# Performance work log

Measured on AMD Instinct MI355X. Metric: run time of the kernel, lower is better.

The kernel has to match this reference:

```python
import jax, jax.numpy as jnp
import numpy as np

B, S, H = 1, 1024, 2880
NQ, NKV, D = 64, 8, 64          # query heads, kv heads, head_dim
G = NQ // NKV                    # GQA group size
W = 128                          # sliding window
SCALE = D ** -0.5
NEG = -1e30


def rotate_half(x):
    x1, x2 = jnp.split(x, 2, axis=-1)
    return jnp.concatenate((-x2, x1), axis=-1)


def setup_inputs() -> dict:
    key = jax.random.key(0)
    ks = jax.random.split(key, 8)
    hidden_states = jax.random.normal(ks[0], (B, S, H), jnp.float32)
    # rotary tables, half head_dim (module concats (cos,cos) to full dim)
    pos = jnp.arange(S, dtype=jnp.float32)[:, None]
    inv = 1.0 / (10000.0 ** (jnp.arange(0, D, 2, dtype=jnp.float32) / D))
    ang = pos * inv[None, :]                      # (S, D/2)
    cos = jnp.cos(ang)[None].astype(jnp.float32)  # (1, S, D/2)
    sin = jnp.sin(ang)[None].astype(jnp.float32)
    w_qkv = jax.random.normal(ks[1], (H, (NQ + 2 * NKV) * D), jnp.float32) * 0.02
    b_qkv = jax.random.normal(ks[2], ((NQ + 2 * NKV) * D,), jnp.float32) * 0.02
    w_o = jax.random.normal(ks[3], (NQ * D, H), jnp.float32) * 0.02
    b_o = jax.random.normal(ks[4], (H,), jnp.float32) * 0.02
    sinks = jax.random.normal(ks[5], (NQ,), jnp.float32)
    k_cache = jnp.zeros((B, S, NKV, D), jnp.float32)
    v_cache = jnp.zeros((B, S, NKV, D), jnp.float32)
    return {"hidden_states": hidden_states, "cos": cos, "sin": sin,
            "w_qkv": w_qkv, "b_qkv": b_qkv, "w_o": w_o, "b_o": b_o,
            "sinks": sinks, "k_cache": k_cache, "v_cache": v_cache, "kv_len": 0}


def reference(hidden_states, cos, sin, w_qkv, b_qkv, w_o, b_o, sinks,
              k_cache, v_cache, kv_len):
    # fused QKV projection + split
    qkv = hidden_states @ w_qkv + b_qkv                      # (B, S, (NQ+2*NKV)*D)
    q, k, v = jnp.split(qkv, [NQ * D, NQ * D + NKV * D], axis=-1)
    q = q.reshape(B, S, NQ, D)
    k = k.reshape(B, S, NKV, D)
    v = v.reshape(B, S, NKV, D)
    # RoPE (BSND layout, half-dim tables duplicated to full dim)
    cosf = jnp.concatenate((cos, cos), axis=-1)[:, :, None, :]
    sinf = jnp.concatenate((sin, sin), axis=-1)[:, :, None, :]
    q = q * cosf + rotate_half(q) * sinf
    k = k * cosf + rotate_half(k) * sinf
    # KV-cache scatter update at position kv_len along seq dim
    k_cache = jax.lax.dynamic_update_slice(k_cache, k, (0, kv_len, 0, 0))
    v_cache = jax.lax.dynamic_update_slice(v_cache, v, (0, kv_len, 0, 0))
    T = kv_len + S
    keys = k_cache[:, :T]                                    # (B, T, NKV, D)
    vals = v_cache[:, :T]
    # GQA: group query heads by kv head
    qg = q.reshape(B, S, NKV, G, D)
    scores = jnp.einsum('bqhgd,bkhd->bhgqk', qg, keys) * SCALE  # (B,NKV,G,S,T)
    # causal + sliding-window mask
    i = jnp.arange(S)[:, None] + kv_len
    j = jnp.arange(T)[None, :]
    allowed = (j <= i) & (i - j < W)
    scores = jnp.where(allowed, scores, NEG)
    # softmax with per-head learnable sink logit (sink gets no value)
    sk = sinks.reshape(NKV, G)[None, :, :, None]             # (1,NKV,G,1)
    m = jnp.maximum(jnp.max(scores, axis=-1), sk)            # (B,NKV,G,S)
    p = jnp.exp(scores - m[..., None])
    denom = jnp.sum(p, axis=-1) + jnp.exp(sk - m)
    attn = jnp.einsum('bhgqk,bkhd->bqhgd', p / denom[..., None], vals)
    out = attn.reshape(B, S, NQ * D) @ w_o + b_o             # (B, S, H)
    return out
```

## Files before the change

### kernel.cpp

```cpp
#include <hip/hip_runtime.h>
#include <hip/hip_bf16.h>

#define NQH 64
#define NKVH 8
#define DH 64
#define SEQ 1024
#define HID 2880
#define QKV_N 5120
#define ATTN_N 4096
#define WIN 128
#define WO_NPAD 2944
#define SCALE_F 0.125f

typedef __attribute__((ext_vector_type(8))) __bf16 bf16x8;
typedef __attribute__((ext_vector_type(4))) float f32x4;

#define GLOAD_LDS16(g, l) \
    __builtin_amdgcn_global_load_lds((const __attribute__((address_space(1))) void*)(g), \
                                     (__attribute__((address_space(3))) void*)(l), 16, 0, 0)

__device__ __forceinline__ ushort f2bf(float x) {
    union { float f; unsigned int u; } c; c.f = x;
    unsigned int u = c.u;
    unsigned int r = (u + 0x7FFFu + ((u >> 16) & 1u)) >> 16;
    return (ushort)r;
}

__global__ __launch_bounds__(256) void convert_f32_bf16(
    const float* __restrict__ in, ushort* __restrict__ out, int n4)
{
    int idx = blockIdx.x * blockDim.x + threadIdx.x;
    int stride = gridDim.x * blockDim.x;
    for (int i = idx; i < n4; i += stride) {
        float4 v = reinterpret_cast<const float4*>(in)[i];
        ushort4 o;
        o.x = f2bf(v.x); o.y = f2bf(v.y); o.z = f2bf(v.z); o.w = f2bf(v.w);
        reinterpret_cast<ushort4*>(out)[i] = o;
    }
}

__global__ __launch_bounds__(256) void transpose_convert(
    const float* __restrict__ in, ushort* __restrict__ out, int K, int N)
{
    __shared__ ushort tile[64][80];
    const int bk = blockIdx.x * 64;
    const int bn = blockIdx.y * 64;
    const int tid = threadIdx.x;
    const bool inb = bn < N;

#pragma unroll
    for (int it = 0; it < 4; ++it) {
        int r = it * 16 + (tid >> 4);
        int c4 = (tid & 15) * 4;
        float4 v = make_float4(0.f, 0.f, 0.f, 0.f);
        if (inb) v = *(const float4*)&in[(size_t)(bk + r) * N + bn + c4];
        tile[c4 + 0][r] = f2bf(v.x);
        tile[c4 + 1][r] = f2bf(v.y);
        tile[c4 + 2][r] = f2bf(v.z);
        tile[c4 + 3][r] = f2bf(v.w);
    }
    __syncthreads();
#pragma unroll
    for (int it = 0; it < 2; ++it) {
        int nr = it * 32 + (tid >> 3);
        int c8 = (tid & 7) * 8;
        uint4 v = *(const uint4*)&tile[nr][c8];
        *(uint4*)&out[(size_t)(bn + nr) * K + bk + c8] = v;
    }
}

template<bool ROPE>
__global__ __launch_bounds__(256) void gemm64x128(
    const ushort* __restrict__ A, const ushort* __restrict__ BT,
    const float* __restrict__ bias, float* __restrict__ C,
    int K, int ldC, int Nreal,
    const float* __restrict__ cosp, const float* __restrict__ sinp)
{
    __shared__ ushort Al[2 * 64 * 64];
    __shared__ ushort Bl[2 * 128 * 64];
    const int t = threadIdx.x;
    const int lane = t & 63;
    const int w = t >> 6;
    const int wr = w >> 1, wc = w & 1;
    const int g4 = lane >> 4;
    const int r15 = lane & 15;

    const int flat = blockIdx.x + gridDim.x * blockIdx.y;
    const int per = (gridDim.x * gridDim.y) >> 3;
    const int virt = (flat & 7) * per + (flat >> 3);
    const int m0 = (virt & 15) * 64;
    const int n0 = (virt >> 4) * 128;

    const ushort* aSrc0; const ushort* aSrc1;
    ushort* aDst0; ushort* aDst1;
    {
        int lin0 = t, lin1 = 256 + t;
        int row0 = lin0 >> 3, row1 = lin1 >> 3;
        int ch0 = (lin0 & 7) ^ (row0 & 7);
        int ch1 = (lin1 & 7) ^ (row1 & 7);
        aSrc0 = A + (size_t)(m0 + row0) * K + ch0 * 8;
        aSrc1 = A + (size_t)(m0 + row1) * K + ch1 * 8;
        aDst0 = &Al[lin0 * 8];
        aDst1 = &Al[lin1 * 8];
    }
    const ushort* bSrc0; const ushort* bSrc1; const ushort* bSrc2; const ushort* bSrc3;
    ushort* bDst0; ushort* bDst1; ushort* bDst2; ushort* bDst3;
    {
        int lin;
        lin = t;       bSrc0 = BT + (size_t)(n0 + (lin >> 3)) * K + (((lin & 7) ^ ((lin >> 3) & 7)) * 8); bDst0 = &Bl[lin * 8];
        lin = 256 + t; bSrc1 = BT + (size_t)(n0 + (lin >> 3)) * K + (((lin & 7) ^ ((lin >> 3) & 7)) * 8); bDst1 = &Bl[lin * 8];
        lin = 512 + t; bSrc2 = BT + (size_t)(n0 + (lin >> 3)) * K + (((lin & 7) ^ ((lin >> 3) & 7)) * 8); bDst2 = &Bl[lin * 8];
        lin = 768 + t; bSrc3 = BT + (size_t)(n0 + (lin >> 3)) * K + (((lin & 7) ^ ((lin >> 3) & 7)) * 8); bDst3 = &Bl[lin * 8];
    }

#define STAGE_TILE(bufsel) do { \
        GLOAD_LDS16(aSrc0, aDst0 + (bufsel) * 4096); \
        GLOAD_LDS16(aSrc1, aDst1 + (bufsel) * 4096); \
        GLOAD_LDS16(bSrc0, bDst0 + (bufsel) * 8192); \
        GLOAD_LDS16(bSrc1, bDst1 + (bufsel) * 8192); \
        GLOAD_LDS16(bSrc2, bDst2 + (bufsel) * 8192); \
        GLOAD_LDS16(bSrc3, bDst3 + (bufsel) * 8192); \
        aSrc0 += 64; aSrc1 += 64; \
        bSrc0 += 64; bSrc1 += 64; bSrc2 += 64; bSrc3 += 64; \
    } while (0)

    int aoff[2][2], boff[4][2];
#pragma unroll
    for (int mi = 0; mi < 2; ++mi)
#pragma unroll
        for (int ks = 0; ks < 2; ++ks) {
            int row = wr * 32 + mi * 16 + r15;
            int slot = (ks * 4 + g4) ^ (row & 7);
            aoff[mi][ks] = row * 64 + slot * 8;
        }
#pragma unroll
    for (int ni = 0; ni < 4; ++ni)
#pragma unroll
        for (int ks = 0; ks < 2; ++ks) {
            int col = wc * 64 + ni * 16 + r15;
            int slot = (ks * 4 + g4) ^ (col & 7);
            boff[ni][ks] = col * 64 + slot * 8;
        }

    f32x4 acc[2][4];
#pragma unroll
    for (int mi = 0; mi < 2; ++mi)
#pragma unroll
        for (int ni = 0; ni < 4; ++ni) acc[mi][ni] = (f32x4){0.f, 0.f, 0.f, 0.f};

#define COMPUTE_TILE(bufsel) do { \
        const ushort* Ab = &Al[(bufsel) * 4096]; \
        const ushort* Bb = &Bl[(bufsel) * 8192]; \
        _Pragma("unroll") \
        for (int ks = 0; ks < 2; ++ks) { \
            bf16x8 a0 = *(const bf16x8*)&Ab[aoff[0][ks]]; \
            bf16x8 a1 = *(const bf16x8*)&Ab[aoff[1][ks]]; \
            bf16x8 b0 = *(const bf16x8*)&Bb[boff[0][ks]]; \
            bf16x8 b1 = *(const bf16x8*)&Bb[boff[1][ks]]; \
            bf16x8 b2 = *(const bf16x8*)&Bb[boff[2][ks]]; \
            bf16x8 b3 = *(const bf16x8*)&Bb[boff[3][ks]]; \
            __builtin_amdgcn_s_setprio(1); \
            acc[0][0] = __builtin_amdgcn_mfma_f32_16x16x32_bf16(a0, b0, acc[0][0], 0, 0, 0); \
            acc[0][1] = __builtin_amdgcn_mfma_f32_16x16x32_bf16(a0, b1, acc[0][1], 0, 0, 0); \
            acc[0][2] = __builtin_amdgcn_mfma_f32_16x16x32_bf16(a0, b2, acc[0][2], 0, 0, 0); \
            acc[0][3] = __builtin_amdgcn_mfma_f32_16x16x32_bf16(a0, b3, acc[0][3], 0, 0, 0); \
            acc[1][0] = __builtin_amdgcn_mfma_f32_16x16x32_bf16(a1, b0, acc[1][0], 0, 0, 0); \
            acc[1][1] = __builtin_amdgcn_mfma_f32_16x16x32_bf16(a1, b1, acc[1][1], 0, 0, 0); \
            acc[1][2] = __builtin_amdgcn_mfma_f32_16x16x32_bf16(a1, b2, acc[1][2], 0, 0, 0); \
            acc[1][3] = __builtin_amdgcn_mfma_f32_16x16x32_bf16(a1, b3, acc[1][3], 0, 0, 0); \
            __builtin_amdgcn_s_setprio(0); \
        } \
    } while (0)

    const int NT = K >> 6;
    STAGE_TILE(0);
    for (int kt = 0; kt < NT; kt += 2) {
        if (kt + 1 < NT) {
            STAGE_TILE(1);
            asm volatile("s_waitcnt vmcnt(6)" ::: "memory");
        } else {
            asm volatile("s_waitcnt vmcnt(0)" ::: "memory");
        }
        __builtin_amdgcn_s_barrier();
        COMPUTE_TILE(0);
        asm volatile("s_waitcnt lgkmcnt(0)" ::: "memory");
        __builtin_amdgcn_s_barrier();
        if (kt + 1 < NT) {
            if (kt + 2 < NT) {
                STAGE_TILE(0);
                asm volatile("s_waitcnt vmcnt(6)" ::: "memory");
            } else {
                asm volatile("s_waitcnt vmcnt(0)" ::: "memory");
            }
            __builtin_amdgcn_s_barrier();
            COMPUTE_TILE(1);
            asm volatile("s_waitcnt lgkmcnt(0)" ::: "memory");
            __builtin_amdgcn_s_barrier();
        }
    }
#undef STAGE_TILE
#undef COMPUTE_TILE

    float vals[2][4][4];
#pragma unroll
    for (int ni = 0; ni < 4; ++ni) {
        int col = n0 + wc * 64 + ni * 16 + r15;
        float bv = (col < Nreal) ? bias[col] : 0.f;
#pragma unroll
        for (int mi = 0; mi < 2; ++mi)
#pragma unroll
            for (int r = 0; r < 4; ++r) vals[mi][ni][r] = acc[mi][ni][r] + bv;
    }
    if (ROPE) {
        const int head = (n0 + wc * 64) >> 6;
        if (head < 72) {
#pragma unroll
            for (int mi = 0; mi < 2; ++mi)
#pragma unroll
                for (int r = 0; r < 4; ++r) {
                    int q = m0 + wr * 32 + mi * 16 + g4 * 4 + r;
#pragma unroll
                    for (int dp = 0; dp < 2; ++dp) {
                        int d = dp * 16 + r15;
                        float c = cosp[q * 32 + d];
                        float s = sinp[q * 32 + d];
                        float x1 = vals[mi][dp][r];
                        float x2 = vals[mi][dp + 2][r];
                        vals[mi][dp][r]     = x1 * c - x2 * s;
                        vals[mi][dp + 2][r] = x2 * c + x1 * s;
                    }
                }
        }
    }
#pragma unroll
    for (int ni = 0; ni < 4; ++ni) {
        int col = n0 + wc * 64 + ni * 16 + r15;
        if (col < Nreal) {
#pragma unroll
            for (int mi = 0; mi < 2; ++mi) {
                int row = m0 + wr * 32 + mi * 16 + g4 * 4;
#pragma unroll
                for (int r = 0; r < 4; ++r)
                    C[(size_t)(row + r) * ldC + col] = vals[mi][ni][r];
            }
        }
    }
}

__global__ __launch_bounds__(512) void attn_mfma_kernel(
    const float* __restrict__ qkv, const float* __restrict__ sinks,
    ushort* __restrict__ attn_out)
{
    __shared__ __align__(16) ushort Kl[160][72];
    __shared__ __align__(16) ushort Vt[64][168];
    __shared__ __align__(16) ushort Pl[8][32][40];
    const int t = threadIdx.x;
    const int w = t >> 6;
    const int l = t & 63;
    const int g4 = l >> 4;
    const int r15 = l & 15;
    const int q0 = blockIdx.x * 32;
    const int hk = blockIdx.y;
    const int kbase = q0 - 128;

#pragma unroll
    for (int i = 0; i < 5; ++i) {
        int idx = i * 512 + t;
        int row = idx >> 4;
        int c4 = (idx & 15) * 4;
        int j = kbase + row;
        float4 kv = make_float4(0.f, 0.f, 0.f, 0.f);
        float4 vv = make_float4(0.f, 0.f, 0.f, 0.f);
        if (j >= 0) {
            kv = *(const float4*)&qkv[(size_t)j * QKV_N + 4096 + hk * 64 + c4];
            vv = *(const float4*)&qkv[(size_t)j * QKV_N + 4608 + hk * 64 + c4];
        }
        ushort4 kp;
        kp.x = f2bf(kv.x); kp.y = f2bf(kv.y); kp.z = f2bf(kv.z); kp.w = f2bf(kv.w);
        *(ushort4*)&Kl[row][c4] = kp;
        Vt[c4 + 0][row] = f2bf(vv.x);
        Vt[c4 + 1][row] = f2bf(vv.y);
        Vt[c4 + 2][row] = f2bf(vv.z);
        Vt[c4 + 3][row] = f2bf(vv.w);
    }

    bf16x8 qf[2][2];
#pragma unroll
    for (int ct = 0; ct < 2; ++ct) {
        int R = w * 32 + ct * 16 + r15;
        int q = q0 + (R & 31);
        int hq = hk * 8 + (R >> 5);
        const float* qb = &qkv[(size_t)q * QKV_N + hq * 64];
#pragma unroll
        for (int s = 0; s < 2; ++s) {
            float4 a = *(const float4*)&qb[s * 32 + g4 * 8];
            float4 b = *(const float4*)&qb[s * 32 + g4 * 8 + 4];
            union { ushort u[8]; bf16x8 v; } pk;
            pk.u[0] = f2bf(a.x * SCALE_F); pk.u[1] = f2bf(a.y * SCALE_F);
            pk.u[2] = f2bf(a.z * SCALE_F); pk.u[3] = f2bf(a.w * SCALE_F);
            pk.u[4] = f2bf(b.x * SCALE_F); pk.u[5] = f2bf(b.y * SCALE_F);
            pk.u[6] = f2bf(b.z * SCALE_F); pk.u[7] = f2bf(b.w * SCALE_F);
            qf[ct][s] = pk.v;
        }
    }
    __syncthreads();

    f32x4 sc[10][2];
#pragma unroll
    for (int kt = 0; kt < 10; ++kt) {
        sc[kt][0] = (f32x4){0.f, 0.f, 0.f, 0.f};
        sc[kt][1] = (f32x4){0.f, 0.f, 0.f, 0.f};
    }
#pragma unroll
    for (int kt = 0; kt < 10; ++kt) {
#pragma unroll
        for (int s = 0; s < 2; ++s) {
            bf16x8 kf = *(const bf16x8*)&Kl[kt * 16 + r15][s * 32 + g4 * 8];
            sc[kt][0] = __builtin_amdgcn_mfma_f32_16x16x32_bf16(kf, qf[0][s], sc[kt][0], 0, 0, 0);
            sc[kt][1] = __builtin_amdgcn_mfma_f32_16x16x32_bf16(kf, qf[1][s], sc[kt][1], 0, 0, 0);
        }
    }

    const int minkey = 128 - q0;
#pragma unroll
    for (int ct = 0; ct < 2; ++ct) {
        int R = w * 32 + ct * 16 + r15;
        int ql = R & 31;
        float snk = sinks[hk * 8 + (R >> 5)];
#pragma unroll
        for (int kt = 0; kt < 10; ++kt)
#pragma unroll
            for (int r = 0; r < 4; ++r) {
                int key = kt * 16 + g4 * 4 + r;
                bool ok = (key > ql) && (key <= ql + 128) && (key >= minkey);
                if (!ok) sc[kt][ct][r] = -1e30f;
            }
        float m = snk;
#pragma unroll
        for (int kt = 0; kt < 10; ++kt)
#pragma unroll
            for (int r = 0; r < 4; ++r) m = fmaxf(m, sc[kt][ct][r]);
        m = fmaxf(m, __shfl_xor(m, 16));
        m = fmaxf(m, __shfl_xor(m, 32));
        float sum = 0.f;
#pragma unroll
        for (int kt = 0; kt < 10; ++kt)
#pragma unroll
            for (int r = 0; r < 4; ++r) {
                float p = __expf(sc[kt][ct][r] - m);
                sc[kt][ct][r] = p;
                sum += p;
            }
        sum += __shfl_xor(sum, 16);
        sum += __shfl_xor(sum, 32);
        sum += __expf(snk - m);
        float iv = 1.0f / sum;
#pragma unroll
        for (int kt = 0; kt < 10; ++kt)
#pragma unroll
            for (int r = 0; r < 4; ++r) sc[kt][ct][r] *= iv;
    }

    f32x4 pv[2][4];
#pragma unroll
    for (int mi = 0; mi < 2; ++mi)
#pragma unroll
        for (int ni = 0; ni < 4; ++ni) pv[mi][ni] = (f32x4){0.f, 0.f, 0.f, 0.f};

#pragma unroll
    for (int s = 0; s < 5; ++s) {
#pragma unroll
        for (int ct = 0; ct < 2; ++ct)
#pragma unroll
            for (int kh = 0; kh < 2; ++kh) {
                int kt = 2 * s + kh;
                ushort4 p4;
                p4.x = f2bf(sc[kt][ct][0]);
                p4.y = f2bf(sc[kt][ct][1]);
                p4.z = f2bf(sc[kt][ct][2]);
                p4.w = f2bf(sc[kt][ct][3]);
                *(ushort4*)&Pl[w][ct * 16 + r15][kh * 16 + g4 * 4] = p4;
            }
#pragma unroll
        for (int mi = 0; mi < 2; ++mi) {
            bf16x8 pf = *(const bf16x8*)&Pl[w][mi * 16 + r15][g4 * 8];
#pragma unroll
            for (int ni = 0; ni < 4; ++ni) {
                bf16x8 vf = *(const bf16x8*)&Vt[ni * 16 + r15][s * 32 + g4 * 8];
                pv[mi][ni] = __builtin_amdgcn_mfma_f32_16x16x32_bf16(pf, vf, pv[mi][ni], 0, 0, 0);
            }
        }
    }

#pragma unroll
    for (int mi = 0; mi < 2; ++mi)
#pragma unroll
        for (int r = 0; r < 4; ++r) {
            int R = w * 32 + mi * 16 + g4 * 4 + r;
            int q = q0 + (R & 31);
            int hq = hk * 8 + (R >> 5);
            ushort* ob = &attn_out[(size_t)q * ATTN_N + hq * 64 + r15];
#pragma unroll
            for (int ni = 0; ni < 4; ++ni)
                ob[ni * 16] = f2bf(pv[mi][ni][r]);
        }
}

extern "C" void kernel_launch(void* const* d_in, const int* in_sizes, int n_in,
                              void* d_out, int out_size, void* d_ws, size_t ws_size,
                              hipStream_t stream)
{
    const float* hidden = (const float*)d_in[0];
    const float* cosp   = (const float*)d_in[1];
    const float* sinp   = (const float*)d_in[2];
    const float* w_qkv  = (const float*)d_in[3];
    const float* b_qkv  = (const float*)d_in[4];
    const float* w_o    = (const float*)d_in[5];
    const float* b_o    = (const float*)d_in[6];
    const float* sinks  = (const float*)d_in[7];

    char* ws = (char*)d_ws;
    size_t off = 0;
    ushort* wqkvT = (ushort*)(ws + off); off += (size_t)QKV_N * HID * 2;
    ushort* woT   = (ushort*)(ws + off); off += (size_t)WO_NPAD * ATTN_N * 2;
    float*  qkv   = (float*)(ws + off);  off += (size_t)SEQ * QKV_N * 4;
    ushort* hidden_b = (ushort*)(ws + off);
    ushort* attn_b   = (ushort*)(ws + off); off += (size_t)SEQ * ATTN_N * 2;
    if (off > ws_size) return;

    transpose_convert<<<dim3(HID / 64, QKV_N / 64), 256, 0, stream>>>(w_qkv, wqkvT, HID, QKV_N);
    transpose_convert<<<dim3(ATTN_N / 64, WO_NPAD / 64), 256, 0, stream>>>(w_o, woT, ATTN_N, HID);
    convert_f32_bf16<<<2048, 256, 0, stream>>>(hidden, hidden_b, SEQ * HID / 4);

    gemm64x128<true><<<dim3(QKV_N / 128, SEQ / 64), 256, 0, stream>>>(
        hidden_b, wqkvT, b_qkv, qkv, HID, QKV_N, QKV_N, cosp, sinp);

    attn_mfma_kernel<<<dim3(SEQ / 32, NKVH), 512, 0, stream>>>(qkv, sinks, attn_b);

    gemm64x128<false><<<dim3(WO_NPAD / 128, SEQ / 64), 256, 0, stream>>>(
        attn_b, woT, b_o, (float*)d_out, ATTN_N, HID, HID, nullptr, nullptr);
}
```

Baseline: 151.9 us.

## Enlarge GEMM block tile to 128x128 with eight waves per block

Both GEMMs now use 128x128 output tiles computed by 512-thread blocks (8 waves, each still 32x64), replacing the 64x128 tile with 4 waves. Each block loads A and B tiles with two LDS-direct loads per operand per thread, which raises reuse of the B tile across more rows. The change also removes s_setprio around the MFMA bursts and inserts sched_barriers around the compute sections. The grid halves in block count, which risks lower occupancy or poorer load balance across CUs, especially for the output projection with 23 column tiles.

```diff
diff --git a/kernel.cpp b/kernel.cpp
--- a/kernel.cpp
+++ b/kernel.cpp
@@ -70,58 +70,48 @@
 }
 
 template<bool ROPE>
-__global__ __launch_bounds__(256) void gemm64x128(
+__global__ __launch_bounds__(512) void gemm128w8(
     const ushort* __restrict__ A, const ushort* __restrict__ BT,
     const float* __restrict__ bias, float* __restrict__ C,
     int K, int ldC, int Nreal,
     const float* __restrict__ cosp, const float* __restrict__ sinp)
 {
-    __shared__ ushort Al[2 * 64 * 64];
-    __shared__ ushort Bl[2 * 128 * 64];
+    __shared__ ushort Al[2 * 8192];
+    __shared__ ushort Bl[2 * 8192];
     const int t = threadIdx.x;
     const int lane = t & 63;
     const int w = t >> 6;
-    const int wr = w >> 1, wc = w & 1;
+    const int wr = w >> 1;
+    const int wc = w & 1;
     const int g4 = lane >> 4;
     const int r15 = lane & 15;
 
     const int flat = blockIdx.x + gridDim.x * blockIdx.y;
     const int per = (gridDim.x * gridDim.y) >> 3;
     const int virt = (flat & 7) * per + (flat >> 3);
-    const int m0 = (virt & 15) * 64;
-    const int n0 = (virt >> 4) * 128;
-
-    const ushort* aSrc0; const ushort* aSrc1;
-    ushort* aDst0; ushort* aDst1;
+    const int m0 = (virt & 7) * 128;
+    const int n0 = (virt >> 3) * 128;
+
+    const ushort *aS0, *aS1, *bS0, *bS1;
+    int dO0, dO1;
     {
-        int lin0 = t, lin1 = 256 + t;
+        int lin0 = t, lin1 = 512 + t;
         int row0 = lin0 >> 3, row1 = lin1 >> 3;
         int ch0 = (lin0 & 7) ^ (row0 & 7);
         int ch1 = (lin1 & 7) ^ (row1 & 7);
-        aSrc0 = A + (size_t)(m0 + row0) * K + ch0 * 8;
-        aSrc1 = A + (size_t)(m0 + row1) * K + ch1 * 8;
-        aDst0 = &Al[lin0 * 8];
-        aDst1 = &Al[lin1 * 8];
-    }
-    const ushort* bSrc0; const ushort* bSrc1; const ushort* bSrc2; const ushort* bSrc3;
-    ushort* bDst0; ushort* bDst1; ushort* bDst2; ushort* bDst3;
-    {
-        int lin;
-        lin = t;       bSrc0 = BT + (size_t)(n0 + (lin >> 3)) * K + (((lin & 7) ^ ((lin >> 3) & 7)) * 8); bDst0 = &Bl[lin * 8];
-        lin = 256 + t; bSrc1 = BT + (size_t)(n0 + (lin >> 3)) * K + (((lin & 7) ^ ((lin >> 3) & 7)) * 8); bDst1 = &Bl[lin * 8];
-        lin = 512 + t; bSrc2 = BT + (size_t)(n0 + (lin >> 3)) * K + (((lin & 7) ^ ((lin >> 3) & 7)) * 8); bDst2 = &Bl[lin * 8];
-        lin = 768 + t; bSrc3 = BT + (size_t)(n0 + (lin >> 3)) * K + (((lin & 7) ^ ((lin >> 3) & 7)) * 8); bDst3 = &Bl[lin * 8];
-    }
-
-#define STAGE_TILE(bufsel) do { \
-        GLOAD_LDS16(aSrc0, aDst0 + (bufsel) * 4096); \
-        GLOAD_LDS16(aSrc1, aDst1 + (bufsel) * 4096); \
-        GLOAD_LDS16(bSrc0, bDst0 + (bufsel) * 8192); \
-        GLOAD_LDS16(bSrc1, bDst1 + (bufsel) * 8192); \
-        GLOAD_LDS16(bSrc2, bDst2 + (bufsel) * 8192); \
-        GLOAD_LDS16(bSrc3, bDst3 + (bufsel) * 8192); \
-        aSrc0 += 64; aSrc1 += 64; \
-        bSrc0 += 64; bSrc1 += 64; bSrc2 += 64; bSrc3 += 64; \
+        aS0 = A  + (size_t)(m0 + row0) * K + ch0 * 8;
+        aS1 = A  + (size_t)(m0 + row1) * K + ch1 * 8;
+        bS0 = BT + (size_t)(n0 + row0) * K + ch0 * 8;
+        bS1 = BT + (size_t)(n0 + row1) * K + ch1 * 8;
+        dO0 = lin0 * 8; dO1 = lin1 * 8;
+    }
+
+#define STAGE_TILE(buf) do { \
+        GLOAD_LDS16(aS0, &Al[(buf) * 8192 + dO0]); \
+        GLOAD_LDS16(aS1, &Al[(buf) * 8192 + dO1]); \
+        GLOAD_LDS16(bS0, &Bl[(buf) * 8192 + dO0]); \
+        GLOAD_LDS16(bS1, &Bl[(buf) * 8192 + dO1]); \
+        aS0 += 64; aS1 += 64; bS0 += 64; bS1 += 64; \
     } while (0)
 
     int aoff[2][2], boff[4][2];
@@ -148,9 +138,9 @@
 #pragma unroll
         for (int ni = 0; ni < 4; ++ni) acc[mi][ni] = (f32x4){0.f, 0.f, 0.f, 0.f};
 
-#define COMPUTE_TILE(bufsel) do { \
-        const ushort* Ab = &Al[(bufsel) * 4096]; \
-        const ushort* Bb = &Bl[(bufsel) * 8192]; \
+#define COMPUTE_TILE(buf) do { \
+        const ushort* Ab = &Al[(buf) * 8192]; \
+        const ushort* Bb = &Bl[(buf) * 8192]; \
         _Pragma("unroll") \
         for (int ks = 0; ks < 2; ++ks) { \
             bf16x8 a0 = *(const bf16x8*)&Ab[aoff[0][ks]]; \
@@ -159,7 +149,6 @@
             bf16x8 b1 = *(const bf16x8*)&Bb[boff[1][ks]]; \
             bf16x8 b2 = *(const bf16x8*)&Bb[boff[2][ks]]; \
             bf16x8 b3 = *(const bf16x8*)&Bb[boff[3][ks]]; \
-            __builtin_amdgcn_s_setprio(1); \
             acc[0][0] = __builtin_amdgcn_mfma_f32_16x16x32_bf16(a0, b0, acc[0][0], 0, 0, 0); \
             acc[0][1] = __builtin_amdgcn_mfma_f32_16x16x32_bf16(a0, b1, acc[0][1], 0, 0, 0); \
             acc[0][2] = __builtin_amdgcn_mfma_f32_16x16x32_bf16(a0, b2, acc[0][2], 0, 0, 0); \
@@ -168,7 +157,6 @@
             acc[1][1] = __builtin_amdgcn_mfma_f32_16x16x32_bf16(a1, b1, acc[1][1], 0, 0, 0); \
             acc[1][2] = __builtin_amdgcn_mfma_f32_16x16x32_bf16(a1, b2, acc[1][2], 0, 0, 0); \
             acc[1][3] = __builtin_amdgcn_mfma_f32_16x16x32_bf16(a1, b3, acc[1][3], 0, 0, 0); \
-            __builtin_amdgcn_s_setprio(0); \
         } \
     } while (0)
 
@@ -177,31 +165,34 @@
     for (int kt = 0; kt < NT; kt += 2) {
         if (kt + 1 < NT) {
             STAGE_TILE(1);
-            asm volatile("s_waitcnt vmcnt(6)" ::: "memory");
+            asm volatile("s_waitcnt vmcnt(4)" ::: "memory");
         } else {
             asm volatile("s_waitcnt vmcnt(0)" ::: "memory");
         }
         __builtin_amdgcn_s_barrier();
+        __builtin_amdgcn_sched_barrier(0);
         COMPUTE_TILE(0);
         asm volatile("s_waitcnt lgkmcnt(0)" ::: "memory");
+        __builtin_amdgcn_sched_barrier(0);
         __builtin_amdgcn_s_barrier();
         if (kt + 1 < NT) {
             if (kt + 2 < NT) {
                 STAGE_TILE(0);
-                asm volatile("s_waitcnt vmcnt(6)" ::: "memory");
+                asm volatile("s_waitcnt vmcnt(4)" ::: "memory");
             } else {
                 asm volatile("s_waitcnt vmcnt(0)" ::: "memory");
             }
             __builtin_amdgcn_s_barrier();
+            __builtin_amdgcn_sched_barrier(0);
             COMPUTE_TILE(1);
             asm volatile("s_waitcnt lgkmcnt(0)" ::: "memory");
+            __builtin_amdgcn_sched_barrier(0);
             __builtin_amdgcn_s_barrier();
         }
     }
 #undef STAGE_TILE
 #undef COMPUTE_TILE
 
-    float vals[2][4][4];
 #pragma unroll
     for (int ni = 0; ni < 4; ++ni) {
         int col = n0 + wc * 64 + ni * 16 + r15;
@@ -209,7 +200,7 @@
 #pragma unroll
         for (int mi = 0; mi < 2; ++mi)
 #pragma unroll
-            for (int r = 0; r < 4; ++r) vals[mi][ni][r] = acc[mi][ni][r] + bv;
+            for (int r = 0; r < 4; ++r) acc[mi][ni][r] += bv;
     }
     if (ROPE) {
         const int head = (n0 + wc * 64) >> 6;
@@ -224,10 +215,10 @@
                         int d = dp * 16 + r15;
                         float c = cosp[q * 32 + d];
                         float s = sinp[q * 32 + d];
-                        float x1 = vals[mi][dp][r];
-                        float x2 = vals[mi][dp + 2][r];
-                        vals[mi][dp][r]     = x1 * c - x2 * s;
-                        vals[mi][dp + 2][r] = x2 * c + x1 * s;
+                        float x1 = acc[mi][dp][r];
+                        float x2 = acc[mi][dp + 2][r];
+                        acc[mi][dp][r]     = x1 * c - x2 * s;
+                        acc[mi][dp + 2][r] = x2 * c + x1 * s;
                     }
                 }
         }
@@ -241,7 +232,7 @@
                 int row = m0 + wr * 32 + mi * 16 + g4 * 4;
 #pragma unroll
                 for (int r = 0; r < 4; ++r)
-                    C[(size_t)(row + r) * ldC + col] = vals[mi][ni][r];
+                    C[(size_t)(row + r) * ldC + col] = acc[mi][ni][r];
             }
         }
     }
@@ -432,11 +423,11 @@
     transpose_convert<<<dim3(ATTN_N / 64, WO_NPAD / 64), 256, 0, stream>>>(w_o, woT, ATTN_N, HID);
     convert_f32_bf16<<<2048, 256, 0, stream>>>(hidden, hidden_b, SEQ * HID / 4);
 
-    gemm64x128<true><<<dim3(QKV_N / 128, SEQ / 64), 256, 0, stream>>>(
+    gemm128w8<true><<<dim3(QKV_N / 128, SEQ / 128), 512, 0, stream>>>(
         hidden_b, wqkvT, b_qkv, qkv, HID, QKV_N, QKV_N, cosp, sinp);
 
     attn_mfma_kernel<<<dim3(SEQ / 32, NKVH), 512, 0, stream>>>(qkv, sinks, attn_b);
 
-    gemm64x128<false><<<dim3(WO_NPAD / 128, SEQ / 64), 256, 0, stream>>>(
+    gemm128w8<false><<<dim3(WO_NPAD / 128, SEQ / 128), 512, 0, stream>>>(
         attn_b, woT, b_o, (float*)d_out, ATTN_N, HID, HID, nullptr, nullptr);
 }
```

Measured after the change: 146.5 us. -3.6%, faster.
